# Kernel tuning notes

Hardware: AMD Instinct MI355X
Metric: run time of the kernel (lower is better)

The kernel has to match this reference:

```python
import jax, jax.numpy as jnp
import numpy as np

H = 1024
VOCAB = 32000


def setup_inputs() -> dict:
    key = jax.random.key(0)
    ks = jax.random.split(key, 16)
    N, B, T = 32, 64, 400
    s = 1.0 / np.sqrt(H)
    inp = {
        "input_seq": jax.random.randint(ks[0], (N, B), 0, VOCAB),
        "last_hidden": jax.random.normal(ks[1], (1, B, H), jnp.float32),
        "encoder_outputs": jax.random.normal(ks[2], (T, B, H), jnp.float32),
        "encoderB_outputs": jax.random.normal(ks[3], (T, B, H), jnp.float32),
        # parameters
        "emb": jax.random.normal(ks[4], (VOCAB, H), jnp.float32),
        "W_ih": jax.random.uniform(ks[5], (3 * H, H), jnp.float32, -s, s),
        "W_hh": jax.random.uniform(ks[6], (3 * H, H), jnp.float32, -s, s),
        "b_ih": jax.random.uniform(ks[7], (3 * H,), jnp.float32, -s, s),
        "b_hh": jax.random.uniform(ks[8], (3 * H,), jnp.float32, -s, s),
        "attn_W": jax.random.uniform(ks[9], (H, 2 * H), jnp.float32, -s, s),
        "attn_b": jax.random.uniform(ks[10], (H,), jnp.float32, -s, s),
        "attn_v": jax.random.uniform(ks[11], (H,), jnp.float32, -s, s),
        "concat_W": jax.random.uniform(ks[12], (H, 3 * H), jnp.float32, -s, s),
        "concat_b": jax.random.uniform(ks[13], (H,), jnp.float32, -s, s),
        "out_W": jax.random.uniform(ks[14], (VOCAB, H), jnp.float32, -s, s),
        "out_b": jax.random.uniform(ks[15], (VOCAB,), jnp.float32, -s, s),
    }
    return inp


def _gru(x, h0, W_ih, W_hh, b_ih, b_hh):
    # x: (N,B,H), h0: (B,H). PyTorch GRU cell equations.
    def step(h, x_t):
        gi = x_t @ W_ih.T + b_ih          # (B,3H)
        gh = h @ W_hh.T + b_hh
        i_r, i_z, i_n = jnp.split(gi, 3, axis=-1)
        h_r, h_z, h_n = jnp.split(gh, 3, axis=-1)
        r = jax.nn.sigmoid(i_r + h_r)
        z = jax.nn.sigmoid(i_z + h_z)
        n = jnp.tanh(i_n + r * h_n)
        h_new = (1.0 - z) * n + z * h
        return h_new, h_new
    hN, outs = jax.lax.scan(step, h0, x)
    return outs, hN


def _attention(rnn_out, enc, attn_W, attn_b, v):
    # score(h, e) = (Linear([h; e]) ) . v  -- linear in both, so separable.
    W1, W2 = attn_W[:, :H], attn_W[:, H:]
    u1 = W1.T @ v                         # (H,)
    u2 = W2.T @ v
    bias = attn_b @ v                     # scalar
    a = rnn_out @ u1                      # (N,B)
    c = enc @ u2 + bias                   # (T,B)
    # energies (B,N,T), softmax over T (matches F.softmax on (-1, max_len))
    e = a.T[:, :, None] + c.T[:, None, :]
    w = jax.nn.softmax(e, axis=-1)        # (B,N,T)
    ctx = jnp.einsum('bnt,tbh->nbh', w, enc)  # bmm then transpose(0,1)
    return w, ctx


def reference(input_seq, last_hidden, encoder_outputs, encoderB_outputs,
              emb, W_ih, W_hh, b_ih, b_hh, attn_W, attn_b, attn_v,
              concat_W, concat_b, out_W, out_b):
    x = emb[input_seq]                                   # (N,B,H)
    rnn_out, hN = _gru(x, last_hidden[0], W_ih, W_hh, b_ih, b_hh)
    hidden = hN[None]                                    # (1,B,H)
    uw, u_ctx = _attention(rnn_out, encoder_outputs, attn_W, attn_b, attn_v)
    bw, b_ctx = _attention(rnn_out, encoderB_outputs, attn_W, attn_b, attn_v)
    cat = jnp.concatenate([rnn_out, u_ctx, b_ctx], axis=2)   # (N,B,3H)
    h = jnp.tanh(cat @ concat_W.T + concat_b)
    output = h @ out_W.T + out_b                          # (N,B,VOCAB)
    return output, hidden, uw, bw
```

## Files before the change

### kernel.cpp

```cpp
#include <hip/hip_runtime.h>
#include <cstdint>
#include <cstddef>

namespace {

constexpr int kH  = 1024;
constexpr int kB  = 64;
constexpr int kN  = 32;
constexpr int kT  = 400;
constexpr int kV  = 32000;
constexpr int kM  = kN * kB;
constexpr int k3H = 3 * kH;

typedef _Float16 f16;
typedef _Float16 f16x4 __attribute__((ext_vector_type(4)));
typedef _Float16 f16x8 __attribute__((ext_vector_type(8)));
typedef float    f32x4v __attribute__((ext_vector_type(4)));

__device__ __forceinline__ void gload_lds16(const void* g, void* l) {
  __builtin_amdgcn_global_load_lds((__attribute__((address_space(1))) void*)g,
                                   (__attribute__((address_space(3))) void*)l,
                                   16, 0, 0);
}

__device__ __forceinline__ uint32_t pack_f16x2(f16 lo, f16 hi) {
  union { f16 h[2]; uint32_t u; } c;
  c.h[0] = lo; c.h[1] = hi;
  return c.u;
}


__global__ __launch_bounds__(256)
void pre_kernel(const float* __restrict__ Wih, f16* __restrict__ WihH,
                const float* __restrict__ Whh, f16* __restrict__ WhhH,
                const int* __restrict__ seq, const float* __restrict__ emb,
                f16* __restrict__ Xh, const float* __restrict__ lh,
                f16* __restrict__ HH0,
                const float* __restrict__ attnW, const float* __restrict__ attnB,
                const float* __restrict__ attnV,
                float* __restrict__ u2, float* __restrict__ biasS) {
  const int bid = blockIdx.x, tid = threadIdx.x;
  if (bid < 512) {
    const float* src = (bid < 256) ? Wih : Whh;
    f16* dst = (bid < 256) ? WihH : WhhH;
    constexpr int n4 = k3H * kH / 4;
    for (int i = (bid & 255) * 256 + tid; i < n4; i += 256 * 256) {
      float4 v = reinterpret_cast<const float4*>(src)[i];
      f16x4 o = { (f16)v.x, (f16)v.y, (f16)v.z, (f16)v.w };
      reinterpret_cast<f16x4*>(dst)[i] = o;
    }
  } else if (bid < 640) {
    const int m0 = (bid - 512) * 16;
    for (int k = 0; k < 16; ++k) {
      const int m = m0 + k;
      const int tok = seq[m];
      float4 v = reinterpret_cast<const float4*>(emb + (size_t)tok * kH)[tid];
      f16x4 o = { (f16)v.x, (f16)v.y, (f16)v.z, (f16)v.w };
      reinterpret_cast<f16x4*>(Xh + (size_t)m * kH)[tid] = o;
    }
  } else if (bid < 644) {
    for (int i = (bid - 640) * 256 + tid; i < 16384; i += 1024) {
      float4 v = reinterpret_cast<const float4*>(lh)[i];
      f16x4 o = { (f16)v.x, (f16)v.y, (f16)v.z, (f16)v.w };
      reinterpret_cast<f16x4*>(HH0)[i] = o;
    }
  } else {
    const int item = (bid - 644) * 4 + (tid >> 6);
    const int lane = tid & 63;
    if (item > kH) return;
    float sum = 0.0f;
    if (item < kH) {
      for (int k = lane; k < kH; k += 64)
        sum += attnW[(size_t)k * (2 * kH) + kH + item] * attnV[k];
    } else {
      for (int k = lane; k < kH; k += 64)
        sum += attnB[k] * attnV[k];
    }
    #pragma unroll
    for (int o = 32; o > 0; o >>= 1) sum += __shfl_xor(sum, o);
    if (lane == 0) { if (item < kH) u2[item] = sum; else biasS[0] = sum; }
  }
}


template <bool TANH, typename OUT_T>
__global__ __launch_bounds__(256, 4)
void gemm_bt_kernel(const f16* __restrict__ A, const f16* __restrict__ Bt,
                    const float* __restrict__ bias, OUT_T* __restrict__ C,
                    int M, int N, int K) {
  __shared__ __align__(16) f16 As[128 * 64];
  __shared__ __align__(16) f16 Bs[128 * 64];
  const int tid  = threadIdx.x;
  const int wave = tid >> 6;
  const int lane = tid & 63;
  const int m0 = blockIdx.x * 128;
  const int n0 = blockIdx.y * 128;
  const int wm = (wave >> 1) * 64;
  const int wn = (wave & 1) * 64;
  const int rsub = lane >> 3;
  const int coff = (lane & 7) * 8;
  f32x4v acc[4][4] = {};
  const int nk = K >> 6;
  for (int kc = 0; kc < nk; ++kc) {
    const f16* Ag = A + (size_t)m0 * K + kc * 64;
    const f16* Bg = Bt + (size_t)n0 * K + kc * 64;
    for (int c = wave; c < 16; c += 4) {
      const int row = c * 8 + rsub;
      gload_lds16(Ag + (size_t)row * K + coff, &As[c * 512]);
      gload_lds16(Bg + (size_t)row * K + coff, &Bs[c * 512]);
    }
    __syncthreads();
    #pragma unroll
    for (int kk = 0; kk < 2; ++kk) {
      const int ko = kk * 32 + (lane >> 4) * 8;
      f16x8 af[4], bfr[4];
      #pragma unroll
      for (int i = 0; i < 4; ++i) {
        af[i]  = *reinterpret_cast<const f16x8*>(&As[(wm + i * 16 + (lane & 15)) * 64 + ko]);
        bfr[i] = *reinterpret_cast<const f16x8*>(&Bs[(wn + i * 16 + (lane & 15)) * 64 + ko]);
      }
      #pragma unroll
      for (int mi = 0; mi < 4; ++mi)
        #pragma unroll
        for (int ni = 0; ni < 4; ++ni)
          acc[mi][ni] = __builtin_amdgcn_mfma_f32_16x16x32_f16(af[mi], bfr[ni], acc[mi][ni], 0, 0, 0);
    }
    __syncthreads();
  }
  const int rb = (lane >> 4) * 4;
  const int cb = lane & 15;
  #pragma unroll
  for (int mi = 0; mi < 4; ++mi) {
    #pragma unroll
    for (int ni = 0; ni < 4; ++ni) {
      const int col = n0 + wn + ni * 16 + cb;
      const float bv = bias[col];
      #pragma unroll
      for (int r = 0; r < 4; ++r) {
        const int row = m0 + wm + mi * 16 + rb + r;
        float v = acc[mi][ni][r] + bv;
        if (TANH) v = tanhf(v);
        C[(size_t)row * N + col] = (OUT_T)v;
      }
    }
  }
}


constexpr int kGruBlks = 64;
constexpr int kAttnBlks = 128;
constexpr int kCvtBlks = 320;
constexpr int kMegaBlks = kGruBlks + kAttnBlks + kCvtBlks;

__global__ __launch_bounds__(256, 1)
void mega_kernel(const f16* __restrict__ Whh, const float* __restrict__ bhh,
                 const float* __restrict__ gi, const float* __restrict__ lh,
                 f16* __restrict__ HHa, f16* __restrict__ HHb,
                 f16* __restrict__ cath, float* __restrict__ hiddenOut,
                 unsigned int* __restrict__ flags,
                 const float* __restrict__ enc0, const float* __restrict__ enc1,
                 const float* __restrict__ u2, const float* __restrict__ biasS,
                 float* __restrict__ uw, float* __restrict__ bw,
                 const float* __restrict__ oW, f16* __restrict__ oWh,
                 const float* __restrict__ cW, f16* __restrict__ cWh) {
  __shared__ union SM {
    float ghp[4][64][52];
    struct { float4 u2s[256]; float srow[kT]; float red[8]; } at;
  } sm;
  const int bid = blockIdx.x;
  const int tid = threadIdx.x;
  const int wave = tid >> 6;
  const int lane = tid & 63;

  if (bid < kGruBlks) {
    const int ln   = lane & 15;
    const int khi  = lane >> 4;
    const int j0   = bid * 16;
    const int kw   = wave * 256;
    const int fm   = tid >> 2;
    const int fc   = (tid & 3) * 4;
    const int myprod = wave * 16 + ln;

    f16x8 bfr[3][8];
    #pragma unroll
    for (int s = 0; s < 3; ++s)
      #pragma unroll
      for (int ks = 0; ks < 8; ++ks)
        bfr[s][ks] = *reinterpret_cast<const f16x8*>(
            &Whh[(size_t)(s * kH + j0 + ln) * kH + kw + ks * 32 + khi * 8]);

    float hreg[4], bR[4], bZ[4], bN[4];
    #pragma unroll
    for (int e = 0; e < 4; ++e) {
      const int j = j0 + fc + e;
      hreg[e] = lh[(size_t)fm * kH + j];
      bR[e] = bhh[j]; bZ[e] = bhh[kH + j]; bN[e] = bhh[2 * kH + j];
    }

    for (int step = 0; step < kN; ++step) {
      const f16* hh  = (step & 1) ? HHb : HHa;
      f16*       hho = (step & 1) ? HHa : HHb;

      float4 giL[3];
      {
        const size_t mm = (size_t)step * kB + fm;
        #pragma unroll
        for (int s = 0; s < 3; ++s)
          giL[s] = *reinterpret_cast<const float4*>(&gi[mm * k3H + s * kH + j0 + fc]);
      }

      if (step > 0) {
        while (true) {
          unsigned int f = __hip_atomic_load(&flags[myprod], __ATOMIC_RELAXED,
                                             __HIP_MEMORY_SCOPE_SYSTEM);
          if (__all(f >= (unsigned int)step)) break;
          __builtin_amdgcn_s_sleep(1);
        }
        __builtin_amdgcn_fence(__ATOMIC_ACQUIRE, "agent");
      }

      f16x8 af[8][4];
      #pragma unroll
      for (int ks = 0; ks < 8; ++ks)
        #pragma unroll
        for (int mi = 0; mi < 4; ++mi)
          af[ks][mi] = *reinterpret_cast<const f16x8*>(
              &hh[(size_t)(mi * 16 + ln) * kH + kw + ks * 32 + khi * 8]);

      f32x4v acc[4][3] = {};
      #pragma unroll
      for (int ks = 0; ks < 8; ++ks)
        #pragma unroll
        for (int mi = 0; mi < 4; ++mi)
          #pragma unroll
          for (int s = 0; s < 3; ++s)
            acc[mi][s] = __builtin_amdgcn_mfma_f32_16x16x32_f16(af[ks][mi], bfr[s][ks], acc[mi][s], 0, 0, 0);

      #pragma unroll
      for (int mi = 0; mi < 4; ++mi)
        #pragma unroll
        for (int s = 0; s < 3; ++s)
          #pragma unroll
          for (int r = 0; r < 4; ++r)
            sm.ghp[wave][mi * 16 + khi * 4 + r][s * 16 + ln] = acc[mi][s][r];
      __syncthreads();

      float4 gr4 = {0,0,0,0}, gz4 = {0,0,0,0}, gn4 = {0,0,0,0};
      #pragma unroll
      for (int w = 0; w < 4; ++w) {
        float4 a = *reinterpret_cast<const float4*>(&sm.ghp[w][fm][fc]);
        float4 b = *reinterpret_cast<const float4*>(&sm.ghp[w][fm][16 + fc]);
        float4 c = *reinterpret_cast<const float4*>(&sm.ghp[w][fm][32 + fc]);
        gr4.x += a.x; gr4.y += a.y; gr4.z += a.z; gr4.w += a.w;
        gz4.x += b.x; gz4.y += b.y; gz4.z += b.z; gz4.w += b.w;
        gn4.x += c.x; gn4.y += c.y; gn4.z += c.z; gn4.w += c.w;
      }
      float hv[4];
      const float* grp = &gr4.x; const float* gzp = &gz4.x; const float* gnp = &gn4.x;
      const float* g0 = &giL[0].x; const float* g1 = &giL[1].x; const float* g2 = &giL[2].x;
      #pragma unroll
      for (int e = 0; e < 4; ++e) {
        const float r  = 1.0f / (1.0f + expf(-(g0[e] + grp[e] + bR[e])));
        const float z  = 1.0f / (1.0f + expf(-(g1[e] + gzp[e] + bZ[e])));
        const float nn = tanhf(g2[e] + r * (gnp[e] + bN[e]));
        hv[e] = (1.0f - z) * nn + z * hreg[e];
        hreg[e] = hv[e];
      }
      const uint32_t p01 = pack_f16x2((f16)hv[0], (f16)hv[1]);
      const uint32_t p23 = pack_f16x2((f16)hv[2], (f16)hv[3]);
      const unsigned long long pk64 = (unsigned long long)p01 | ((unsigned long long)p23 << 32);
      __hip_atomic_store(reinterpret_cast<unsigned long long*>(&hho[(size_t)fm * kH + j0 + fc]),
                         pk64, __ATOMIC_RELAXED, __HIP_MEMORY_SCOPE_AGENT);
      __syncthreads();
      if (step < kN - 1 && tid == 0)
        __hip_atomic_store(&flags[bid], (unsigned int)(step + 1),
                           __ATOMIC_RELAXED, __HIP_MEMORY_SCOPE_SYSTEM);
      uint2 pku; pku.x = p01; pku.y = p23;
      *reinterpret_cast<uint2*>(&cath[((size_t)step * kB + fm) * k3H + j0 + fc]) = pku;
      if (step == kN - 1) {
        float4 hv4 = { hv[0], hv[1], hv[2], hv[3] };
        *reinterpret_cast<float4*>(&hiddenOut[(size_t)fm * kH + j0 + fc]) = hv4;
      }
    }
  } else if (bid < kGruBlks + kAttnBlks) {
    const int idx = bid - kGruBlks;
    const int e = idx >> 6, b = idx & 63;
    const float* enc = e ? enc1 : enc0;

    sm.at.u2s[tid] = *reinterpret_cast<const float4*>(&u2[tid * 4]);
    __syncthreads();
    const float bias = biasS[0];

    for (int t = wave; t < kT; t += 4) {
      const float* row = enc + ((size_t)t * kB + b) * kH + lane * 16;
      float s = 0.0f;
      #pragma unroll
      for (int i = 0; i < 4; ++i) {
        float4 ev = reinterpret_cast<const float4*>(row)[i];
        float4 uv = sm.at.u2s[lane * 4 + i];
        s += ev.x * uv.x + ev.y * uv.y + ev.z * uv.z + ev.w * uv.w;
      }
      #pragma unroll
      for (int o = 32; o > 0; o >>= 1) s += __shfl_xor(s, o);
      if (lane == 0) sm.at.srow[t] = s + bias;
    }
    __syncthreads();

    float lmax = -1e30f;
    for (int t = tid; t < kT; t += 256) lmax = fmaxf(lmax, sm.at.srow[t]);
    #pragma unroll
    for (int o = 32; o > 0; o >>= 1) lmax = fmaxf(lmax, __shfl_xor(lmax, o));
    if (lane == 0) sm.at.red[wave] = lmax;
    __syncthreads();
    const float m = fmaxf(fmaxf(sm.at.red[0], sm.at.red[1]), fmaxf(sm.at.red[2], sm.at.red[3]));
    float lsum = 0.0f;
    for (int t = tid; t < kT; t += 256) {
      float ev = expf(sm.at.srow[t] - m);
      sm.at.srow[t] = ev;
      lsum += ev;
    }
    #pragma unroll
    for (int o = 32; o > 0; o >>= 1) lsum += __shfl_xor(lsum, o);
    if (lane == 0) sm.at.red[4 + wave] = lsum;
    __syncthreads();
    const float inv = 1.0f / (sm.at.red[4] + sm.at.red[5] + sm.at.red[6] + sm.at.red[7]);
    for (int t = tid; t < kT; t += 256) sm.at.srow[t] *= inv;
    __syncthreads();

    float* outp = (e ? bw : uw) + (size_t)b * kN * kT;
    for (int n = 0; n < kN; ++n)
      for (int t = tid; t < kT; t += 256)
        __builtin_nontemporal_store(sm.at.srow[t], &outp[n * kT + t]);

    const int j = tid * 4;
    float4 acc = {0,0,0,0};
    for (int t = 0; t < kT; ++t) {
      const float wt = sm.at.srow[t];
      const float4 ev = *reinterpret_cast<const float4*>(&enc[((size_t)t * kB + b) * kH + j]);
      acc.x += wt * ev.x; acc.y += wt * ev.y; acc.z += wt * ev.z; acc.w += wt * ev.w;
    }
    f16x4 cv = { (f16)acc.x, (f16)acc.y, (f16)acc.z, (f16)acc.w };
    #pragma unroll
    for (int n = 0; n < kN; ++n)
      *reinterpret_cast<f16x4*>(&cath[((size_t)(n * kB + b)) * k3H + kH + e * kH + j]) = cv;
  } else {
    constexpr int nOW = kV * kH / 4;
    constexpr int nCW = kH * k3H / 4;
    const int stride = kCvtBlks * 256;
    for (int i = (bid - kGruBlks - kAttnBlks) * 256 + tid; i < nOW + nCW; i += stride) {
      if (i < nOW) {
        float4 v = reinterpret_cast<const float4*>(oW)[i];
        f16x4 o = { (f16)v.x, (f16)v.y, (f16)v.z, (f16)v.w };
        reinterpret_cast<f16x4*>(oWh)[i] = o;
      } else {
        const int k = i - nOW;
        float4 v = reinterpret_cast<const float4*>(cW)[k];
        f16x4 o = { (f16)v.x, (f16)v.y, (f16)v.z, (f16)v.w };
        reinterpret_cast<f16x4*>(cWh)[k] = o;
      }
    }
  }
}

}


extern "C" void kernel_launch(void* const* d_in, const int* in_sizes, int n_in,
                              void* d_out, int out_size, void* d_ws, size_t ws_size,
                              hipStream_t stream) {
  (void)in_sizes; (void)n_in; (void)out_size; (void)ws_size;
  const int*   seq    = (const int*)d_in[0];
  const float* lh     = (const float*)d_in[1];
  const float* enc0   = (const float*)d_in[2];
  const float* enc1   = (const float*)d_in[3];
  const float* emb    = (const float*)d_in[4];
  const float* W_ih   = (const float*)d_in[5];
  const float* W_hh   = (const float*)d_in[6];
  const float* b_ih   = (const float*)d_in[7];
  const float* b_hh   = (const float*)d_in[8];
  const float* attn_W = (const float*)d_in[9];
  const float* attn_b = (const float*)d_in[10];
  const float* attn_v = (const float*)d_in[11];
  const float* cW     = (const float*)d_in[12];
  const float* cb     = (const float*)d_in[13];
  const float* oW     = (const float*)d_in[14];
  const float* ob     = (const float*)d_in[15];
  float* out = (float*)d_out;

  char* ws = (char*)d_ws;
  constexpr size_t oWih = 0;
  constexpr size_t oWhh = oWih + 6291456;
  constexpr size_t oCW  = oWhh + 6291456;
  constexpr size_t oOW  = oCW + 6291456;
  constexpr size_t oX   = oOW + 65536000;
  constexpr size_t oGI  = oX + 4194304;
  constexpr size_t oHH0 = oGI + 25165824;
  constexpr size_t oHH1 = oHH0 + 131072;
  constexpr size_t oCAT = oHH1 + 131072;
  constexpr size_t oH2  = oCAT + 12582912;
  constexpr size_t oU2  = oH2 + 4194304;
  constexpr size_t oBS  = oU2 + 4096;
  constexpr size_t oCTR = oBS + 256;

  f16*   Wih_h = (f16*)(ws + oWih);
  f16*   Whh_h = (f16*)(ws + oWhh);
  f16*   cW_h  = (f16*)(ws + oCW);
  f16*   oW_h  = (f16*)(ws + oOW);
  f16*   X_h   = (f16*)(ws + oX);
  float* GI    = (float*)(ws + oGI);
  f16*   HH0   = (f16*)(ws + oHH0);
  f16*   HH1   = (f16*)(ws + oHH1);
  f16*   CAT   = (f16*)(ws + oCAT);
  f16*   H2    = (f16*)(ws + oH2);
  float* U2    = (float*)(ws + oU2);
  float* BS    = (float*)(ws + oBS);
  unsigned int* FLAGS = (unsigned int*)(ws + oCTR);

  constexpr size_t oHidden = (size_t)kM * kV;
  constexpr size_t oUW = oHidden + (size_t)kB * kH;
  constexpr size_t oBW = oUW + (size_t)kB * kN * kT;

  pre_kernel<<<901, 256, 0, stream>>>(W_ih, Wih_h, W_hh, Whh_h, seq, emb, X_h,
                                      lh, HH0, attn_W, attn_b, attn_v, U2, BS);
  (void)hipMemsetAsync(FLAGS, 0, 64 * sizeof(unsigned int), stream);

  gemm_bt_kernel<false, float><<<dim3(16, 24), 256, 0, stream>>>(X_h, Wih_h, b_ih, GI, kM, k3H, kH);

  mega_kernel<<<kMegaBlks, 256, 0, stream>>>(Whh_h, b_hh, GI, lh, HH0, HH1, CAT,
                                             out + oHidden, FLAGS,
                                             enc0, enc1, U2, BS,
                                             out + oUW, out + oBW,
                                             oW, oW_h, cW, cW_h);

  gemm_bt_kernel<true, f16><<<dim3(16, 8), 256, 0, stream>>>(CAT, cW_h, cb, H2, kM, kH, k3H);
  gemm_bt_kernel<false, float><<<dim3(16, 250), 256, 0, stream>>>(H2, oW_h, ob, out, kM, kV, kH);
}
```

Measured before the change: 634.4 us.

## Fuse concat and output GEMMs into one persistent kernel with row-flag dependencies

Merges the concat GEMM (tanh) and the vocab projection GEMM into a single persistent kernel. Output tiles for a row block start as soon as that block's eight concat tiles have signalled through a counter, so the two stages can overlap instead of waiting at a kernel boundary. It also splits the attention u2 reduction into a parallel k-chunked form that accumulates with atomics into a zeroed counter area. The costs are spin-waiting and reliance on the scheduling order of blocks to avoid deadlock, plus nondeterministic float atomic sums.

```diff
diff --git a/kernel.cpp b/kernel.cpp
--- a/kernel.cpp
+++ b/kernel.cpp
@@ -29,6 +29,11 @@
   return c.u;
 }
 
+constexpr int C_FLAGS = 0;
+constexpr int C_CONC  = 64;
+constexpr int C_U2    = 640;
+constexpr int C_BS    = 1664;
+
 
 __global__ __launch_bounds__(256)
 void pre_kernel(const float* __restrict__ Wih, f16* __restrict__ WihH,
@@ -37,8 +42,7 @@
                 f16* __restrict__ Xh, const float* __restrict__ lh,
                 f16* __restrict__ HH0,
                 const float* __restrict__ attnW, const float* __restrict__ attnB,
-                const float* __restrict__ attnV,
-                float* __restrict__ u2, float* __restrict__ biasS) {
+                const float* __restrict__ attnV, unsigned int* __restrict__ ctr) {
   const int bid = blockIdx.x, tid = threadIdx.x;
   if (bid < 512) {
     const float* src = (bid < 256) ? Wih : Whh;
@@ -64,37 +68,35 @@
       f16x4 o = { (f16)v.x, (f16)v.y, (f16)v.z, (f16)v.w };
       reinterpret_cast<f16x4*>(HH0)[i] = o;
     }
+  } else if (bid < 708) {
+    const int b  = bid - 644;
+    const int hc = b & 3;
+    const int kc = b >> 2;
+    const int h  = hc * 256 + tid;
+    float sum = 0.0f;
+    for (int k = kc * 64; k < kc * 64 + 64; ++k)
+      sum += attnW[(size_t)k * (2 * kH) + kH + h] * attnV[k];
+    atomicAdd(reinterpret_cast<float*>(ctr + C_U2) + h, sum);
   } else {
-    const int item = (bid - 644) * 4 + (tid >> 6);
-    const int lane = tid & 63;
-    if (item > kH) return;
-    float sum = 0.0f;
-    if (item < kH) {
-      for (int k = lane; k < kH; k += 64)
-        sum += attnW[(size_t)k * (2 * kH) + kH + item] * attnV[k];
-    } else {
-      for (int k = lane; k < kH; k += 64)
-        sum += attnB[k] * attnV[k];
-    }
-    #pragma unroll
-    for (int o = 32; o > 0; o >>= 1) sum += __shfl_xor(sum, o);
-    if (lane == 0) { if (item < kH) u2[item] = sum; else biasS[0] = sum; }
+    if (tid < 64) {
+      float s = 0.0f;
+      for (int k = tid; k < kH; k += 64) s += attnB[k] * attnV[k];
+      #pragma unroll
+      for (int o = 32; o > 0; o >>= 1) s += __shfl_xor(s, o);
+      if (tid == 0) atomicAdd(reinterpret_cast<float*>(ctr + C_BS), s);
+    }
   }
 }
 
 
-template <bool TANH, typename OUT_T>
-__global__ __launch_bounds__(256, 4)
-void gemm_bt_kernel(const f16* __restrict__ A, const f16* __restrict__ Bt,
-                    const float* __restrict__ bias, OUT_T* __restrict__ C,
-                    int M, int N, int K) {
-  __shared__ __align__(16) f16 As[128 * 64];
-  __shared__ __align__(16) f16 Bs[128 * 64];
+template <int MODE>
+__device__ void tile_gemm(f16* __restrict__ As, f16* __restrict__ Bs,
+                          const f16* __restrict__ Ag0, const f16* __restrict__ Bg0,
+                          const float* __restrict__ bias, void* __restrict__ Cout,
+                          int N, int K, int m0, int n0) {
   const int tid  = threadIdx.x;
   const int wave = tid >> 6;
   const int lane = tid & 63;
-  const int m0 = blockIdx.x * 128;
-  const int n0 = blockIdx.y * 128;
   const int wm = (wave >> 1) * 64;
   const int wn = (wave & 1) * 64;
   const int rsub = lane >> 3;
@@ -102,8 +104,8 @@
   f32x4v acc[4][4] = {};
   const int nk = K >> 6;
   for (int kc = 0; kc < nk; ++kc) {
-    const f16* Ag = A + (size_t)m0 * K + kc * 64;
-    const f16* Bg = Bt + (size_t)n0 * K + kc * 64;
+    const f16* Ag = Ag0 + kc * 64;
+    const f16* Bg = Bg0 + kc * 64;
     for (int c = wave; c < 16; c += 4) {
       const int row = c * 8 + rsub;
       gload_lds16(Ag + (size_t)row * K + coff, &As[c * 512]);
@@ -129,20 +131,91 @@
   }
   const int rb = (lane >> 4) * 4;
   const int cb = lane & 15;
-  #pragma unroll
-  for (int mi = 0; mi < 4; ++mi) {
-    #pragma unroll
-    for (int ni = 0; ni < 4; ++ni) {
-      const int col = n0 + wn + ni * 16 + cb;
-      const float bv = bias[col];
-      #pragma unroll
-      for (int r = 0; r < 4; ++r) {
-        const int row = m0 + wm + mi * 16 + rb + r;
-        float v = acc[mi][ni][r] + bv;
-        if (TANH) v = tanhf(v);
-        C[(size_t)row * N + col] = (OUT_T)v;
-      }
-    }
+  if (MODE == 0) {
+    f16* tile = As;
+    #pragma unroll
+    for (int mi = 0; mi < 4; ++mi)
+      #pragma unroll
+      for (int ni = 0; ni < 4; ++ni) {
+        const int col = wn + ni * 16 + cb;
+        const float bv = bias[n0 + col];
+        #pragma unroll
+        for (int r = 0; r < 4; ++r)
+          tile[(wm + mi * 16 + rb + r) * 128 + col] = (f16)tanhf(acc[mi][ni][r] + bv);
+      }
+    __syncthreads();
+    f16* H2 = (f16*)Cout;
+    const int row = tid >> 1;
+    const int c0  = (tid & 1) * 64;
+    #pragma unroll
+    for (int i = 0; i < 16; ++i) {
+      union { f16x4 v; unsigned long long u; } cv;
+      cv.v = *reinterpret_cast<const f16x4*>(&tile[row * 128 + c0 + i * 4]);
+      __hip_atomic_store(reinterpret_cast<unsigned long long*>(
+          &H2[(size_t)(m0 + row) * kH + n0 + c0 + i * 4]),
+          cv.u, __ATOMIC_RELAXED, __HIP_MEMORY_SCOPE_AGENT);
+    }
+  } else {
+    float* C = (float*)Cout;
+    #pragma unroll
+    for (int mi = 0; mi < 4; ++mi)
+      #pragma unroll
+      for (int ni = 0; ni < 4; ++ni) {
+        const int col = n0 + wn + ni * 16 + cb;
+        const float bv = bias[col];
+        #pragma unroll
+        for (int r = 0; r < 4; ++r)
+          C[(size_t)(m0 + wm + mi * 16 + rb + r) * N + col] = acc[mi][ni][r] + bv;
+      }
+  }
+}
+
+
+__global__ __launch_bounds__(256, 4)
+void gemm_bt_kernel(const f16* __restrict__ A, const f16* __restrict__ Bt,
+                    const float* __restrict__ bias, float* __restrict__ C,
+                    int M, int N, int K) {
+  __shared__ __align__(16) f16 sb[2 * 128 * 64];
+  tile_gemm<1>(sb, sb + 8192, A + (size_t)(blockIdx.x * 128) * K,
+               Bt + (size_t)(blockIdx.y * 128) * K, bias, C, N, K,
+               blockIdx.x * 128, blockIdx.y * 128);
+}
+
+
+__global__ __launch_bounds__(256, 4)
+void concat_out_kernel(const f16* __restrict__ CAT, const f16* __restrict__ cWh,
+                       const float* __restrict__ cb, f16* __restrict__ H2,
+                       const f16* __restrict__ oWh, const float* __restrict__ ob,
+                       float* __restrict__ outC, unsigned int* __restrict__ ctr) {
+  __shared__ __align__(16) f16 sb[2 * 128 * 64];
+  f16* As = sb;
+  f16* Bs = sb + 8192;
+  const int tid = threadIdx.x;
+  for (int item = blockIdx.x; item < 4128; item += 1024) {
+    if (item < 128) {
+      const int r  = item & 15;
+      const int ct = item >> 4;
+      tile_gemm<0>(As, Bs, CAT + (size_t)(128 * r) * k3H, cWh + (size_t)(128 * ct) * k3H,
+                   cb, H2, kH, k3H, 128 * r, 128 * ct);
+      __syncthreads();
+      if (tid == 0)
+        __hip_atomic_fetch_add(&ctr[C_CONC + 32 * r], 1u,
+                               __ATOMIC_RELAXED, __HIP_MEMORY_SCOPE_SYSTEM);
+    } else {
+      const int j  = item - 128;
+      const int r  = j & 15;
+      const int ct = j >> 4;
+      if (tid == 0) {
+        while (__hip_atomic_load(&ctr[C_CONC + 32 * r], __ATOMIC_RELAXED,
+                                 __HIP_MEMORY_SCOPE_SYSTEM) < 8u)
+          __builtin_amdgcn_s_sleep(16);
+      }
+      __syncthreads();
+      __builtin_amdgcn_fence(__ATOMIC_ACQUIRE, "agent");
+      tile_gemm<1>(As, Bs, H2 + (size_t)(128 * r) * kH, oWh + (size_t)(128 * ct) * kH,
+                   ob, outC, kV, kH, 128 * r, 128 * ct);
+    }
+    __syncthreads();
   }
 }
 
@@ -398,9 +471,7 @@
   constexpr size_t oHH1 = oHH0 + 131072;
   constexpr size_t oCAT = oHH1 + 131072;
   constexpr size_t oH2  = oCAT + 12582912;
-  constexpr size_t oU2  = oH2 + 4194304;
-  constexpr size_t oBS  = oU2 + 4096;
-  constexpr size_t oCTR = oBS + 256;
+  constexpr size_t oCTR = oH2 + 4194304;
 
   f16*   Wih_h = (f16*)(ws + oWih);
   f16*   Whh_h = (f16*)(ws + oWhh);
@@ -412,26 +483,25 @@
   f16*   HH1   = (f16*)(ws + oHH1);
   f16*   CAT   = (f16*)(ws + oCAT);
   f16*   H2    = (f16*)(ws + oH2);
-  float* U2    = (float*)(ws + oU2);
-  float* BS    = (float*)(ws + oBS);
-  unsigned int* FLAGS = (unsigned int*)(ws + oCTR);
+  unsigned int* CTR = (unsigned int*)(ws + oCTR);
+  float* U2    = (float*)(CTR + C_U2);
+  float* BS    = (float*)(CTR + C_BS);
 
   constexpr size_t oHidden = (size_t)kM * kV;
   constexpr size_t oUW = oHidden + (size_t)kB * kH;
   constexpr size_t oBW = oUW + (size_t)kB * kN * kT;
 
-  pre_kernel<<<901, 256, 0, stream>>>(W_ih, Wih_h, W_hh, Whh_h, seq, emb, X_h,
-                                      lh, HH0, attn_W, attn_b, attn_v, U2, BS);
-  (void)hipMemsetAsync(FLAGS, 0, 64 * sizeof(unsigned int), stream);
-
-  gemm_bt_kernel<false, float><<<dim3(16, 24), 256, 0, stream>>>(X_h, Wih_h, b_ih, GI, kM, k3H, kH);
+  (void)hipMemsetAsync(CTR, 0, 8192, stream);
+  pre_kernel<<<709, 256, 0, stream>>>(W_ih, Wih_h, W_hh, Whh_h, seq, emb, X_h,
+                                      lh, HH0, attn_W, attn_b, attn_v, CTR);
+
+  gemm_bt_kernel<<<dim3(16, 24), 256, 0, stream>>>(X_h, Wih_h, b_ih, GI, kM, k3H, kH);
 
   mega_kernel<<<kMegaBlks, 256, 0, stream>>>(Whh_h, b_hh, GI, lh, HH0, HH1, CAT,
-                                             out + oHidden, FLAGS,
+                                             out + oHidden, CTR,
                                              enc0, enc1, U2, BS,
                                              out + oUW, out + oBW,
                                              oW, oW_h, cW, cW_h);
 
-  gemm_bt_kernel<true, f16><<<dim3(16, 8), 256, 0, stream>>>(CAT, cW_h, cb, H2, kM, kH, k3H);
-  gemm_bt_kernel<false, float><<<dim3(16, 250), 256, 0, stream>>>(H2, oW_h, ob, out, kM, kV, kH);
-}
+  concat_out_kernel<<<1024, 256, 0, stream>>>(CAT, cW_h, cb, H2, oW_h, ob, out, CTR);
+}
```

After: 702.9 us. +10.8%, slower.
